# Optimization experiments

Measured on AMD Instinct MI355X. Metric: run time of the kernel, lower is better.

## Reference

```python
import jax, jax.numpy as jnp
import numpy as np

N_NODES = 50000
N_EDGES = 1600000
IN_FEAT = 128
OUT_FEAT = 128
NUM_RELS = 8


def setup_inputs() -> dict:
    key = jax.random.key(0)
    k1, k2, k3, k4, k5, k6, k7 = jax.random.split(key, 7)
    x = jax.random.normal(k1, (N_NODES, IN_FEAT), dtype=jnp.float32)
    norm = jax.random.uniform(k2, (N_EDGES, 1), dtype=jnp.float32)
    src = jax.random.randint(k3, (N_EDGES,), 0, N_NODES)
    dst = jax.random.randint(k4, (N_EDGES,), 0, N_NODES)
    rel_type = jax.random.randint(k5, (N_EDGES,), 0, NUM_RELS)
    # Xavier-uniform-like init for the relation weight tensor (gain for relu)
    gain = float(np.sqrt(2.0))
    bound = gain * float(np.sqrt(6.0 / (IN_FEAT + OUT_FEAT)))
    weight = jax.random.uniform(k6, (NUM_RELS, IN_FEAT, OUT_FEAT), dtype=jnp.float32,
                                minval=-bound, maxval=bound)
    bias = jax.random.uniform(k7, (OUT_FEAT,), dtype=jnp.float32, minval=-0.1, maxval=0.1)
    return {"x": x, "norm": norm, "weight": weight, "bias": bias,
            "src": src, "dst": dst, "rel_type": rel_type}


def reference(x, norm, weight, bias, src, dst, rel_type):
    n_nodes = x.shape[0]
    # Transform every node feature by every relation matrix: [R, N, O].
    # This is equivalent math to the per-edge bmm(h_src, W[rel]) but avoids
    # materializing an [E, in, out] gathered weight tensor.
    hw = jnp.einsum('ni,rio->rno', x, weight)
    # Per-edge message: gather transformed src feature for edge's relation, scale by norm.
    msg = hw[rel_type, src] * norm            # [E, O]
    # Scatter-sum messages to destination nodes.
    h = jax.ops.segment_sum(msg, dst, num_segments=n_nodes)  # [N, O]
    h = jax.nn.relu(h + bias)
    return h
```

## Files before the change

### kernel.cpp

```cpp
#include <hip/hip_runtime.h>
#include <hip/hip_bf16.h>

typedef unsigned short u16;
typedef unsigned int u32;
typedef u16 u16x4 __attribute__((ext_vector_type(4)));
typedef u16 u16x8 __attribute__((ext_vector_type(8)));
typedef short bf16x8 __attribute__((ext_vector_type(8)));
typedef float f32x4 __attribute__((ext_vector_type(4)));

static __device__ __forceinline__ u16 f32_to_bf16(float f) {
    u32 b = __float_as_uint(f);
    u32 r = (b + 0x7fffu + ((b >> 16) & 1u)) >> 16;
    return (u16)r;
}
static __device__ __forceinline__ float bflo(u32 u) { return __uint_as_float(u << 16); }
static __device__ __forceinline__ float bfhi(u32 u) { return __uint_as_float(u & 0xffff0000u); }

static __device__ __forceinline__ void gload_lds16(const void* g, void* l) {
    __builtin_amdgcn_global_load_lds((const __attribute__((address_space(1))) u32*)g,
                                     (__attribute__((address_space(3))) u32*)l, 16, 0, 0);
}

__global__ __launch_bounds__(256) void k_cvt_x(const float* __restrict__ x, u16* __restrict__ xb, int n) {
    int i = (blockIdx.x * 256 + threadIdx.x) * 4;
    if (i < n) {
        const float4 v = *reinterpret_cast<const float4*>(x + i);
        u16x4 o = { f32_to_bf16(v.x), f32_to_bf16(v.y), f32_to_bf16(v.z), f32_to_bf16(v.w) };
        *reinterpret_cast<u16x4*>(xb + i) = o;
    }
}

__global__ __launch_bounds__(256) void k_cvt_w(const float* __restrict__ w, u16* __restrict__ wtb, int total) {
    int idx = blockIdx.x * 256 + threadIdx.x;
    if (idx < total) {
        int r = idx >> 14, rem = idx & 16383, o = rem >> 7, i = rem & 127;
        wtb[idx] = f32_to_bf16(w[(r << 14) + (i << 7) + o]);
    }
}

__global__ __launch_bounds__(256) void k_histrank(const int* __restrict__ dst, const int* __restrict__ rel,
                                                  int* __restrict__ counts, u32* __restrict__ keyrank, int E) {
    int e = blockIdx.x * 256 + threadIdx.x;
    if (e < E) {
        int b = dst[e] * 8 + rel[e];
        u32 r = (u32)atomicAdd(&counts[b], 1);
        if (r > 255u) r = 255u;
        keyrank[e] = ((u32)b << 8) | r;
    }
}

__global__ __launch_bounds__(256) void k_scan1v(const int* __restrict__ counts, int* __restrict__ offsets,
                                                int* __restrict__ bsum, int n) {
    __shared__ int wsum[4];
    int tid = threadIdx.x;
    int base = blockIdx.x * 8192 + tid * 32;
    int4 c[8];
    const int4* cp = reinterpret_cast<const int4*>(counts + base);
#pragma unroll
    for (int j = 0; j < 8; ++j) c[j] = cp[j];
    int t = 0;
#pragma unroll
    for (int j = 0; j < 8; ++j) t += c[j].x + c[j].y + c[j].z + c[j].w;
    int lane = tid & 63, wid = tid >> 6;
    int s = t;
#pragma unroll
    for (int off = 1; off < 64; off <<= 1) {
        int v = __shfl_up(s, off, 64);
        if (lane >= off) s += v;
    }
    if (lane == 63) wsum[wid] = s;
    __syncthreads();
    int woff = 0;
    for (int wq = 0; wq < wid; ++wq) woff += wsum[wq];
    int run = woff + s - t;
    int4* op = reinterpret_cast<int4*>(offsets + base);
#pragma unroll
    for (int j = 0; j < 8; ++j) {
        int4 o;
        o.x = run; run += c[j].x;
        o.y = run; run += c[j].y;
        o.z = run; run += c[j].z;
        o.w = run; run += c[j].w;
        op[j] = o;
    }
    if (tid == 255) bsum[blockIdx.x] = woff + s;
}

__global__ void k_scan2(const int* __restrict__ bsum, int* __restrict__ bo, int* __restrict__ offsets,
                        int nb, int n) {
    int lane = threadIdx.x;
    int v = (lane < nb) ? bsum[lane] : 0;
    int s = v;
#pragma unroll
    for (int off = 1; off < 64; off <<= 1) {
        int u = __shfl_up(s, off, 64);
        if (lane >= off) s += u;
    }
    if (lane < nb) bo[lane] = s - v;
    if (lane == 63) offsets[n] = s;
}

__global__ __launch_bounds__(256) void k_scan3v(int* __restrict__ offsets, const int* __restrict__ bo, int n4) {
    int i = blockIdx.x * 256 + threadIdx.x;
    if (i < n4) {
        int4 v = reinterpret_cast<int4*>(offsets)[i];
        int b = bo[i >> 11];
        v.x += b; v.y += b; v.z += b; v.w += b;
        reinterpret_cast<int4*>(offsets)[i] = v;
    }
}

__global__ __launch_bounds__(256) void k_fill3(const int* __restrict__ src, const float* __restrict__ norm,
                                               const u32* __restrict__ keyrank, const int* __restrict__ offs,
                                               uint2* __restrict__ meta, int E) {
    int e = blockIdx.x * 256 + threadIdx.x;
    if (e < E) {
        u32 kr = keyrank[e];
        int b = (int)(kr >> 8), r = (int)(kr & 255u);
        meta[offs[b] + r] = make_uint2((u32)src[e], __float_as_uint(norm[e]));
    }
}

__global__ __launch_bounds__(256) void k_aggx(const uint2* __restrict__ meta, const int* __restrict__ offs,
                                              const u16* __restrict__ xb, u16* __restrict__ agg,
                                              int M, int E) {
    int node = blockIdx.x * 4 + (threadIdx.x >> 6);
    if (node >= M) return;
    int lane = threadIdx.x & 63;
    const int ob = node * 8;
    u32* dstp = reinterpret_cast<u32*>(agg + ((size_t)node << 10));
    int ov[9];
#pragma unroll
    for (int i = 0; i < 9; ++i) ov[i] = offs[ob + i];
    const int emax = E - 1;
#pragma unroll
    for (int rp = 0; rp < 8; rp += 2) {
        int eA = ov[rp],     endA = ov[rp + 1];
        int eB = ov[rp + 1], endB = ov[rp + 2];
        float a0 = 0.f, a1 = 0.f, a2 = 0.f, a3 = 0.f;
        float b0 = 0.f, b1 = 0.f, b2 = 0.f, b3 = 0.f;
        while (eA < endA || eB < endB) {
            uint2 mA[4], mB[4];
#pragma unroll
            for (int j = 0; j < 4; ++j) {
                int ia = eA + j, ib = eB + j;
                uint2 a = meta[min(ia, emax)];
                uint2 b = meta[min(ib, emax)];
                if (ia >= endA) a.y = 0u;
                if (ib >= endB) b.y = 0u;
                mA[j] = a; mB[j] = b;
            }
            u32 xA[4], xB[4];
#pragma unroll
            for (int j = 0; j < 4; ++j) {
                xA[j] = reinterpret_cast<const u32*>(xb + ((size_t)mA[j].x << 7))[lane];
                xB[j] = reinterpret_cast<const u32*>(xb + ((size_t)mB[j].x << 7))[lane];
            }
#pragma unroll
            for (int j = 0; j < 4; ++j) {
                float nA = __uint_as_float(mA[j].y), nB = __uint_as_float(mB[j].y);
                if (j & 1) {
                    a2 = fmaf(nA, bflo(xA[j]), a2); a3 = fmaf(nA, bfhi(xA[j]), a3);
                    b2 = fmaf(nB, bflo(xB[j]), b2); b3 = fmaf(nB, bfhi(xB[j]), b3);
                } else {
                    a0 = fmaf(nA, bflo(xA[j]), a0); a1 = fmaf(nA, bfhi(xA[j]), a1);
                    b0 = fmaf(nB, bflo(xB[j]), b0); b1 = fmaf(nB, bfhi(xB[j]), b1);
                }
            }
            eA += 4; eB += 4;
        }
        u32 pkA = (u32)f32_to_bf16(a0 + a2) | ((u32)f32_to_bf16(a1 + a3) << 16);
        u32 pkB = (u32)f32_to_bf16(b0 + b2) | ((u32)f32_to_bf16(b1 + b3) << 16);
        dstp[rp * 64 + lane] = pkA;
        dstp[(rp + 1) * 64 + lane] = pkB;
    }
}

__global__ __launch_bounds__(256) void k_gemm2(const u16* __restrict__ agg, const u16* __restrict__ wtb,
                                               const float* __restrict__ bias, float* __restrict__ out, int M) {
    __shared__ u16 As[128 * 128];
    __shared__ u16 Bs[128 * 128];
    const int tid = threadIdx.x;
    const int lane = tid & 63, wid = tid >> 6;
    const int m0 = blockIdx.x * 128;
    const int wm = wid >> 1, wn = wid & 1;
    const int l16 = lane & 15, kg = lane >> 4;
    f32x4 acc[4][4];
#pragma unroll
    for (int a = 0; a < 4; ++a)
#pragma unroll
        for (int b = 0; b < 4; ++b) acc[a][b] = {0.f, 0.f, 0.f, 0.f};

#pragma unroll 1
    for (int g = 0; g < 8; ++g) {
#pragma unroll
        for (int it = 0; it < 8; ++it) {
            int cb = (it * 4 + wid) * 64;
            int c = cb + lane;
            int row = c >> 4;
            int ch = (c & 15) ^ (row & 7);
            int grow = m0 + row;
            if (grow >= M) grow = M - 1;
            gload_lds16(agg + (((size_t)grow << 10) + (g << 7) + (ch << 3)), &As[cb * 8]);
            gload_lds16(wtb + ((g << 14) + (row << 7) + (ch << 3)), &Bs[cb * 8]);
        }
        __syncthreads();
#pragma unroll
        for (int ks = 0; ks < 4; ++ks) {
            const int kb = ks * 32 + kg * 8;
            bf16x8 af[4], bfr[4];
#pragma unroll
            for (int fi = 0; fi < 4; ++fi) {
                int row = wm * 64 + fi * 16 + l16;
                af[fi] = *reinterpret_cast<const bf16x8*>(&As[row * 128 + (kb ^ ((row & 7) << 3))]);
            }
#pragma unroll
            for (int fj = 0; fj < 4; ++fj) {
                int row = wn * 64 + fj * 16 + l16;
                bfr[fj] = *reinterpret_cast<const bf16x8*>(&Bs[row * 128 + (kb ^ ((row & 7) << 3))]);
            }
#pragma unroll
            for (int fi = 0; fi < 4; ++fi)
#pragma unroll
                for (int fj = 0; fj < 4; ++fj)
                    acc[fi][fj] = __builtin_amdgcn_mfma_f32_16x16x32_bf16(af[fi], bfr[fj], acc[fi][fj], 0, 0, 0);
        }
        __syncthreads();
    }
    float bv[4];
#pragma unroll
    for (int fj = 0; fj < 4; ++fj) bv[fj] = bias[wn * 64 + fj * 16 + l16];
#pragma unroll
    for (int fi = 0; fi < 4; ++fi) {
#pragma unroll
        for (int j = 0; j < 4; ++j) {
            int gr = m0 + wm * 64 + fi * 16 + kg * 4 + j;
            if (gr < M) {
                float* rowp = out + (((size_t)gr << 7) + wn * 64 + l16);
#pragma unroll
                for (int fj = 0; fj < 4; ++fj)
                    rowp[fj * 16] = fmaxf(acc[fi][fj][j] + bv[fj], 0.f);
            }
        }
    }
}

extern "C" void kernel_launch(void* const* d_in, const int* in_sizes, int n_in,
                              void* d_out, int out_size, void* d_ws, size_t ws_size,
                              hipStream_t stream) {
    const float* x    = (const float*)d_in[0];
    const float* norm = (const float*)d_in[1];
    const float* w    = (const float*)d_in[2];
    const float* bias = (const float*)d_in[3];
    const int* src    = (const int*)d_in[4];
    const int* dst    = (const int*)d_in[5];
    const int* rel    = (const int*)d_in[6];
    float* out = (float*)d_out;

    const int M = in_sizes[0] / 128;
    const int E = in_sizes[1];
    const int R = 8;
    const int n2 = M * R;
    const int nb = (n2 + 8191) / 8192;
    const int n2p = nb * 8192;

    char* p = (char*)d_ws;
    auto carve = [&p](size_t bytes) -> char* {
        char* r = p;
        p += (bytes + 255) & ~(size_t)255;
        return r;
    };
    u16* xb      = (u16*)carve((size_t)M * 128 * 2);
    u16* wtb     = (u16*)carve((size_t)R * 128 * 128 * 2);
    int* cnt     = (int*)carve((size_t)n2p * 4);
    int* offs    = (int*)carve((size_t)(n2p + 4) * 4);
    int* bsum    = (int*)carve(512);
    int* bo      = (int*)carve(512);
    uint2* meta  = (uint2*)carve((size_t)E * 8);
    u16* agg     = (u16*)carve((size_t)M * 1024 * 2);
    u32* keyrank = (u32*)agg;

    hipMemsetAsync(cnt, 0, (size_t)n2p * 4, stream);
    k_cvt_x<<<dim3((M * 128 / 4 + 255) / 256), 256, 0, stream>>>(x, xb, M * 128);
    k_cvt_w<<<dim3((R * 128 * 128 + 255) / 256), 256, 0, stream>>>(w, wtb, R * 128 * 128);
    k_histrank<<<dim3((E + 255) / 256), 256, 0, stream>>>(dst, rel, cnt, keyrank, E);
    k_scan1v<<<dim3(nb), 256, 0, stream>>>(cnt, offs, bsum, n2p);
    k_scan2<<<dim3(1), 64, 0, stream>>>(bsum, bo, offs, nb, n2p);
    k_scan3v<<<dim3((n2p / 4 + 255) / 256), 256, 0, stream>>>(offs, bo, n2p / 4);
    k_fill3<<<dim3((E + 255) / 256), 256, 0, stream>>>(src, norm, keyrank, offs, meta, E);
    k_aggx<<<dim3((M + 3) / 4), 256, 0, stream>>>(meta, offs, xb, agg, M, E);
    k_gemm2<<<dim3((M + 127) / 128), 256, 0, stream>>>(agg, wtb, bias, out, M);
    (void)ws_size; (void)n_in; (void)out_size;
}
```

Before: 351.0 us.

## Merge prep kernels into one launch and widen aggregation to four relations

Three small preprocessing kernels (x conversion, weight transpose-convert, histogram/rank) are folded into one launch that picks its role from the block index, removing two launch gaps. The aggregation kernel now walks four relation segments at once in two passes instead of two segments in four passes, issuing 16 independent gathers per iteration to raise memory-level parallelism. This costs more registers and may lower occupancy.

```diff
diff --git a/kernel.cpp b/kernel.cpp
--- a/kernel.cpp
+++ b/kernel.cpp
@@ -21,31 +21,33 @@
                                      (__attribute__((address_space(3))) u32*)l, 16, 0, 0);
 }
 
-__global__ __launch_bounds__(256) void k_cvt_x(const float* __restrict__ x, u16* __restrict__ xb, int n) {
-    int i = (blockIdx.x * 256 + threadIdx.x) * 4;
-    if (i < n) {
-        const float4 v = *reinterpret_cast<const float4*>(x + i);
-        u16x4 o = { f32_to_bf16(v.x), f32_to_bf16(v.y), f32_to_bf16(v.z), f32_to_bf16(v.w) };
-        *reinterpret_cast<u16x4*>(xb + i) = o;
-    }
-}
-
-__global__ __launch_bounds__(256) void k_cvt_w(const float* __restrict__ w, u16* __restrict__ wtb, int total) {
-    int idx = blockIdx.x * 256 + threadIdx.x;
-    if (idx < total) {
-        int r = idx >> 14, rem = idx & 16383, o = rem >> 7, i = rem & 127;
-        wtb[idx] = f32_to_bf16(w[(r << 14) + (i << 7) + o]);
-    }
-}
-
-__global__ __launch_bounds__(256) void k_histrank(const int* __restrict__ dst, const int* __restrict__ rel,
-                                                  int* __restrict__ counts, u32* __restrict__ keyrank, int E) {
-    int e = blockIdx.x * 256 + threadIdx.x;
-    if (e < E) {
-        int b = dst[e] * 8 + rel[e];
-        u32 r = (u32)atomicAdd(&counts[b], 1);
-        if (r > 255u) r = 255u;
-        keyrank[e] = ((u32)b << 8) | r;
+__global__ __launch_bounds__(256) void k_prep(const int* __restrict__ dst, const int* __restrict__ rel,
+                                              int* __restrict__ counts, u32* __restrict__ keyrank, int E,
+                                              const float* __restrict__ x, u16* __restrict__ xb, int nx,
+                                              const float* __restrict__ w, u16* __restrict__ wtb, int nw,
+                                              int nbh, int nbx) {
+    int bid = blockIdx.x;
+    if (bid < nbh) {
+        int e = bid * 256 + threadIdx.x;
+        if (e < E) {
+            int b = dst[e] * 8 + rel[e];
+            u32 r = (u32)atomicAdd(&counts[b], 1);
+            if (r > 255u) r = 255u;
+            keyrank[e] = ((u32)b << 8) | r;
+        }
+    } else if (bid < nbh + nbx) {
+        int i = ((bid - nbh) * 256 + threadIdx.x) * 4;
+        if (i < nx) {
+            const float4 v = *reinterpret_cast<const float4*>(x + i);
+            u16x4 o = { f32_to_bf16(v.x), f32_to_bf16(v.y), f32_to_bf16(v.z), f32_to_bf16(v.w) };
+            *reinterpret_cast<u16x4*>(xb + i) = o;
+        }
+    } else {
+        int idx = (bid - nbh - nbx) * 256 + threadIdx.x;
+        if (idx < nw) {
+            int r = idx >> 14, rem = idx & 16383, o = rem >> 7, i = rem & 127;
+            wtb[idx] = f32_to_bf16(w[(r << 14) + (i << 7) + o]);
+        }
     }
 }
 
@@ -124,55 +126,60 @@
 __global__ __launch_bounds__(256) void k_aggx(const uint2* __restrict__ meta, const int* __restrict__ offs,
                                               const u16* __restrict__ xb, u16* __restrict__ agg,
                                               int M, int E) {
-    int node = blockIdx.x * 4 + (threadIdx.x >> 6);
+    const int wid4 = __builtin_amdgcn_readfirstlane(threadIdx.x >> 6);
+    const int node = blockIdx.x * 4 + wid4;
     if (node >= M) return;
-    int lane = threadIdx.x & 63;
-    const int ob = node * 8;
+    const int lane4 = (threadIdx.x & 63) << 2;
+    const int lane = threadIdx.x & 63;
+    const char* xbb = (const char*)xb;
+    const int emax = E - 1;
     u32* dstp = reinterpret_cast<u32*>(agg + ((size_t)node << 10));
     int ov[9];
 #pragma unroll
-    for (int i = 0; i < 9; ++i) ov[i] = offs[ob + i];
-    const int emax = E - 1;
-#pragma unroll
-    for (int rp = 0; rp < 8; rp += 2) {
-        int eA = ov[rp],     endA = ov[rp + 1];
-        int eB = ov[rp + 1], endB = ov[rp + 2];
-        float a0 = 0.f, a1 = 0.f, a2 = 0.f, a3 = 0.f;
-        float b0 = 0.f, b1 = 0.f, b2 = 0.f, b3 = 0.f;
-        while (eA < endA || eB < endB) {
-            uint2 mA[4], mB[4];
-#pragma unroll
-            for (int j = 0; j < 4; ++j) {
-                int ia = eA + j, ib = eB + j;
-                uint2 a = meta[min(ia, emax)];
-                uint2 b = meta[min(ib, emax)];
-                if (ia >= endA) a.y = 0u;
-                if (ib >= endB) b.y = 0u;
-                mA[j] = a; mB[j] = b;
+    for (int i = 0; i < 9; ++i) ov[i] = offs[node * 8 + i];
+
+#pragma unroll 1
+    for (int pass = 0; pass < 2; ++pass) {
+        int e[4], en[4];
+#pragma unroll
+        for (int s = 0; s < 4; ++s) { e[s] = ov[pass * 4 + s]; en[s] = ov[pass * 4 + s + 1]; }
+        float a0[4], a1[4], a2[4], a3[4];
+#pragma unroll
+        for (int s = 0; s < 4; ++s) { a0[s] = 0.f; a1[s] = 0.f; a2[s] = 0.f; a3[s] = 0.f; }
+
+        while (e[0] < en[0] || e[1] < en[1] || e[2] < en[2] || e[3] < en[3]) {
+            u32 srow[16], nbits[16];
+#pragma unroll
+            for (int s = 0; s < 4; ++s)
+#pragma unroll
+                for (int j = 0; j < 4; ++j) {
+                    int ia = e[s] + j;
+                    uint2 m = meta[min(ia, emax)];
+                    bool ok = ia < en[s];
+                    srow[s * 4 + j] = ok ? m.x : 0u;
+                    nbits[s * 4 + j] = ok ? m.y : 0u;
+                }
+            u32 xv[16];
+#pragma unroll
+            for (int k = 0; k < 16; ++k)
+                xv[k] = *(const u32*)(xbb + ((size_t)srow[k] << 8) + lane4);
+#pragma unroll
+            for (int s = 0; s < 4; ++s) {
+#pragma unroll
+                for (int j = 0; j < 4; ++j) {
+                    float n = __uint_as_float(nbits[s * 4 + j]);
+                    u32 v = xv[s * 4 + j];
+                    if (j & 1) { a2[s] = fmaf(n, bflo(v), a2[s]); a3[s] = fmaf(n, bfhi(v), a3[s]); }
+                    else       { a0[s] = fmaf(n, bflo(v), a0[s]); a1[s] = fmaf(n, bfhi(v), a1[s]); }
+                }
+                e[s] += 4;
             }
-            u32 xA[4], xB[4];
-#pragma unroll
-            for (int j = 0; j < 4; ++j) {
-                xA[j] = reinterpret_cast<const u32*>(xb + ((size_t)mA[j].x << 7))[lane];
-                xB[j] = reinterpret_cast<const u32*>(xb + ((size_t)mB[j].x << 7))[lane];
-            }
-#pragma unroll
-            for (int j = 0; j < 4; ++j) {
-                float nA = __uint_as_float(mA[j].y), nB = __uint_as_float(mB[j].y);
-                if (j & 1) {
-                    a2 = fmaf(nA, bflo(xA[j]), a2); a3 = fmaf(nA, bfhi(xA[j]), a3);
-                    b2 = fmaf(nB, bflo(xB[j]), b2); b3 = fmaf(nB, bfhi(xB[j]), b3);
-                } else {
-                    a0 = fmaf(nA, bflo(xA[j]), a0); a1 = fmaf(nA, bfhi(xA[j]), a1);
-                    b0 = fmaf(nB, bflo(xB[j]), b0); b1 = fmaf(nB, bfhi(xB[j]), b1);
-                }
-            }
-            eA += 4; eB += 4;
-        }
-        u32 pkA = (u32)f32_to_bf16(a0 + a2) | ((u32)f32_to_bf16(a1 + a3) << 16);
-        u32 pkB = (u32)f32_to_bf16(b0 + b2) | ((u32)f32_to_bf16(b1 + b3) << 16);
-        dstp[rp * 64 + lane] = pkA;
-        dstp[(rp + 1) * 64 + lane] = pkB;
+        }
+#pragma unroll
+        for (int s = 0; s < 4; ++s) {
+            u32 pk = (u32)f32_to_bf16(a0[s] + a2[s]) | ((u32)f32_to_bf16(a1[s] + a3[s]) << 16);
+            dstp[(pass * 4 + s) * 64 + lane] = pk;
+        }
     }
 }
 
@@ -280,10 +287,14 @@
     u16* agg     = (u16*)carve((size_t)M * 1024 * 2);
     u32* keyrank = (u32*)agg;
 
+    const int nbh = (E + 255) / 256;
+    const int nbx = (M * 128 / 4 + 255) / 256;
+    const int nbw = (R * 128 * 128 + 255) / 256;
+
     hipMemsetAsync(cnt, 0, (size_t)n2p * 4, stream);
-    k_cvt_x<<<dim3((M * 128 / 4 + 255) / 256), 256, 0, stream>>>(x, xb, M * 128);
-    k_cvt_w<<<dim3((R * 128 * 128 + 255) / 256), 256, 0, stream>>>(w, wtb, R * 128 * 128);
-    k_histrank<<<dim3((E + 255) / 256), 256, 0, stream>>>(dst, rel, cnt, keyrank, E);
+    k_prep<<<dim3(nbh + nbx + nbw), 256, 0, stream>>>(dst, rel, cnt, keyrank, E,
+                                                      x, xb, M * 128, w, wtb, R * 128 * 128,
+                                                      nbh, nbx);
     k_scan1v<<<dim3(nb), 256, 0, stream>>>(cnt, offs, bsum, n2p);
     k_scan2<<<dim3(1), 64, 0, stream>>>(bsum, bo, offs, nb, n2p);
     k_scan3v<<<dim3((n2p / 4 + 255) / 256), 256, 0, stream>>>(offs, bo, n2p / 4);
```

Result: faster. 341.8 us (-2.6%).
